# Kernel tuning notes

Hardware: AMD Instinct MI355X
Metric: run time of the kernel (lower is better)

## Reference

```python
import jax, jax.numpy as jnp
import numpy as np

SCALE = 1.0  # noise std used in the Gaussian log-pdf
HIGH = jax.lax.Precision.HIGHEST


def setup_inputs() -> dict:
    key = jax.random.key(0)
    k1, k2, k3 = jax.random.split(key, 3)
    B, N, D, T = 64, 256, 64, 4096
    data = jax.random.normal(k1, (B, N, D), dtype=jnp.float32)
    targets = jax.random.normal(k2, (B, N), dtype=jnp.float32)
    task_pool = jax.random.normal(k3, (T, D, 1), dtype=jnp.float32)
    return {"data": data, "targets": targets, "task_pool": task_pool}


def reference(data, targets, task_pool):
    # data: [B, N, D], targets: [B, N], task_pool: [T, D, 1]
    W = jnp.squeeze(task_pool).T  # [D, T]
    # Per-point, per-task Gaussian log-likelihood of targets under each task weight.
    Z = jnp.einsum('bnd,dt->bnt', data, W, precision=HIGH)  # [B, N, T]
    resid = targets[:, :, None] - Z
    logp = jax.scipy.stats.norm.logpdf(resid, loc=0.0, scale=SCALE)  # [B, N, T]
    # alpha for step i (i >= 1) is the cumulative log-lik over points 0..i-1.
    cum = jnp.cumsum(logp, axis=1)          # [B, N, T]
    alphas = cum[:, :-1]                    # [B, N-1, T], alphas[:, i-1] = alpha at step i
    post = jax.nn.softmax(alphas, axis=-1)  # posterior over tasks per step
    # MMSE weight per step: posterior-weighted average of task weights.
    w_mmse = jnp.einsum('bit,dt->bid', post, W, precision=HIGH)  # [B, N-1, D]
    preds_rest = jnp.einsum('bid,bid->bi', data[:, 1:], w_mmse)  # [B, N-1]
    # Step 0: prior mean weight (uniform average over task pool).
    pred0 = data[:, 0] @ W.mean(axis=1)  # [B]
    return jnp.concatenate([pred0[:, None], preds_rest], axis=1)  # [B, N]
```

## Files before the change

### kernel.cpp

```cpp
#include <hip/hip_runtime.h>
#include <math.h>

#define BB 64
#define NN 256
#define DD 64
#define TT 4096

#define NCH 16
#define CT (TT/NCH)
#define THREADS 512
#define WAVES 8
#define NB 32
#define NGRP (NN/NB)
#define BN (BB*NN)

#define NHL2E (-0.72134752044448170368f)

typedef __bf16 bf16x4 __attribute__((ext_vector_type(4)));
typedef __bf16 bf16x8 __attribute__((ext_vector_type(8)));
typedef float  f32x4  __attribute__((ext_vector_type(4)));

#define SHR1 0x111
#define SHR2 0x112
#define SHR4 0x114
#define SHR8 0x118

template<int C>
__device__ __forceinline__ float dppf(float x) {
  return __int_as_float(__builtin_amdgcn_update_dpp(
      0, __float_as_int(x), C, 0xf, 0xf, true));
}

__device__ __forceinline__ float bcast15(float x) {
  return __int_as_float(__builtin_amdgcn_ds_swizzle(__float_as_int(x), 0x1F0));
}

#define GLOAD_LDS16(gp, lp_) \
  __builtin_amdgcn_global_load_lds((const __attribute__((address_space(1))) void*)(gp), \
                                   (__attribute__((address_space(3))) void*)(lp_), 16, 0, 0)

__device__ __forceinline__ void merge32(const float2 (*sb)[NB], int lane,
                                        float2* __restrict__ part, size_t obase) {
  const int col = lane & 31;
  float2 p0 = sb[0][col];
  float M = p0.x, S = 1.f, V = p0.y;
  #pragma unroll
  for (int w = 1; w < WAVES; ++w) {
    float2 pw = sb[w][col];
    float mn = fmaxf(M, pw.x);
    float ea = __builtin_amdgcn_exp2f(M - mn);
    float eb = __builtin_amdgcn_exp2f(pw.x - mn);
    S = S * ea + eb;
    V = fmaf(V, ea, pw.y * eb);
    M = mn;
  }
  if (lane < 32) {
    float2 lr;
    lr.x = M + __log2f(S);
    lr.y = V / S;
    part[obase + (size_t)col * NCH] = lr;
  }
}

__global__ __launch_bounds__(THREADS, 4)
void mmse_phase1(const float* __restrict__ data,
                 const float* __restrict__ targets,
                 const float* __restrict__ Wp,
                 float2* __restrict__ part)
{
  const int bx   = blockIdx.x;
  const int b    = bx >> 4;
  const int ch   = bx & 15;
  const int tid  = threadIdx.x;
  const int lane = tid & 63;
  const int wave = tid >> 6;

  __shared__ uint4  dbufq[2][512];
  __shared__ float  tgl[NN];
  __shared__ float2 sbuf[2][WAVES][NB];

  unsigned char* dbufc = (unsigned char*)dbufq;

  bf16x8 aH[2][2], aL[2][2];
  {
    const int tb = ch * CT + wave * 32;
    #pragma unroll
    for (int tile = 0; tile < 2; ++tile) {
      #pragma unroll
      for (int s = 0; s < 2; ++s) {
        const int row = tb + tile * 16 + (lane & 15);
        const int kb  = s * 32 + (lane >> 4) * 8;
        const float* wp = Wp + (size_t)row * DD + kb;
        const float4 qa = *(const float4*)wp;
        const float4 qb = *(const float4*)(wp + 4);
        float f[8] = {qa.x, qa.y, qa.z, qa.w, qb.x, qb.y, qb.z, qb.w};
        bf16x8 hv, lv;
        #pragma unroll
        for (int j = 0; j < 8; ++j) {
          const __bf16 hj = (__bf16)f[j];
          hv[j] = hj;
          lv[j] = (__bf16)(f[j] - (float)hj);
        }
        aH[tile][s] = hv; aL[tile][s] = lv;
      }
    }
  }

  if (wave == 0)
    GLOAD_LDS16(targets + (size_t)b * NN + lane * 4, tgl);

  const float* __restrict__ dbase = data + (size_t)b * NN * DD;
  const int sn  = tid >> 4;
  const int sk8 = tid & 15;
  const int sphys = (sn * 128 + sk8 * 8) ^ ((sn & 7) << 4);

  {
    const float4 q = *(const float4*)(dbase + (size_t)sn * DD + sk8 * 4);
    float f[4] = {q.x, q.y, q.z, q.w};
    bf16x4 hv, lv;
    #pragma unroll
    for (int j = 0; j < 4; ++j) {
      const __bf16 hj = (__bf16)f[j];
      hv[j] = hj;
      lv[j] = (__bf16)(f[j] - (float)hj);
    }
    *(bf16x4*)(dbufc + sphys)        = hv;
    *(bf16x4*)(dbufc + 4096 + sphys) = lv;
  }
  __syncthreads();

  float c8[8];
  #pragma unroll
  for (int i = 0; i < 8; ++i) c8[i] = 0.f;

  const size_t obase0 = (size_t)(b * NN) * NCH + ch;
  const int ra = ((lane & 15) * 128 + (lane >> 4) * 16) ^ ((lane & 7) << 4);

  #pragma unroll 1
  for (int g = 0; g < NGRP; ++g) {
    const int buf = g & 1;
    const unsigned char* bp = dbufc + buf * 8192;

    float4 q;
    if (g + 1 < NGRP)
      q = *(const float4*)(dbase + (size_t)((g + 1) * NB + sn) * DD + sk8 * 4);

    if (g > 0 && wave == ((g - 1) & 7))
      merge32(sbuf[(g - 1) & 1], lane, part, obase0 + (size_t)((g - 1) * NB) * NCH);

    #pragma unroll
    for (int h = 0; h < 2; ++h) {
      const unsigned char* hp = bp + h * 2048;
      bf16x8 bh0 = *(const bf16x8*)(hp + ra);
      bf16x8 bh1 = *(const bf16x8*)(hp + (ra ^ 64));
      bf16x8 bl0 = *(const bf16x8*)(hp + 4096 + ra);
      bf16x8 bl1 = *(const bf16x8*)(hp + 4096 + (ra ^ 64));

      f32x4 zz[2];
      zz[0] = (f32x4)(0.f); zz[1] = (f32x4)(0.f);
      __builtin_amdgcn_s_setprio(1);
      zz[0] = __builtin_amdgcn_mfma_f32_16x16x32_bf16(aH[0][0], bh0, zz[0], 0, 0, 0);
      zz[0] = __builtin_amdgcn_mfma_f32_16x16x32_bf16(aH[0][0], bl0, zz[0], 0, 0, 0);
      zz[0] = __builtin_amdgcn_mfma_f32_16x16x32_bf16(aL[0][0], bh0, zz[0], 0, 0, 0);
      zz[0] = __builtin_amdgcn_mfma_f32_16x16x32_bf16(aH[0][1], bh1, zz[0], 0, 0, 0);
      zz[0] = __builtin_amdgcn_mfma_f32_16x16x32_bf16(aH[0][1], bl1, zz[0], 0, 0, 0);
      zz[0] = __builtin_amdgcn_mfma_f32_16x16x32_bf16(aL[0][1], bh1, zz[0], 0, 0, 0);
      zz[1] = __builtin_amdgcn_mfma_f32_16x16x32_bf16(aH[1][0], bh0, zz[1], 0, 0, 0);
      zz[1] = __builtin_amdgcn_mfma_f32_16x16x32_bf16(aH[1][0], bl0, zz[1], 0, 0, 0);
      zz[1] = __builtin_amdgcn_mfma_f32_16x16x32_bf16(aL[1][0], bh0, zz[1], 0, 0, 0);
      zz[1] = __builtin_amdgcn_mfma_f32_16x16x32_bf16(aH[1][1], bh1, zz[1], 0, 0, 0);
      zz[1] = __builtin_amdgcn_mfma_f32_16x16x32_bf16(aH[1][1], bl1, zz[1], 0, 0, 0);
      zz[1] = __builtin_amdgcn_mfma_f32_16x16x32_bf16(aL[1][1], bh1, zz[1], 0, 0, 0);
      __builtin_amdgcn_s_setprio(0);

      const float tgf = tgl[g * NB + h * 16 + (lane & 15)];

      float alpha[8];
      float mloc = -3.4e38f;
      #pragma unroll
      for (int tile = 0; tile < 2; ++tile) {
        #pragma unroll
        for (int r = 0; r < 4; ++r) {
          const int t8 = tile * 4 + r;
          const float z  = zz[tile][r];
          const float rr = tgf - z;
          const float lp = rr * rr * NHL2E;
          float x = lp;
          x += dppf<SHR1>(x);
          x += dppf<SHR2>(x);
          x += dppf<SHR4>(x);
          x += dppf<SHR8>(x);
          const float tot = bcast15(x);
          const float a_ = c8[t8] + (x - lp);
          alpha[t8] = a_;
          c8[t8] += tot;
          mloc = fmaxf(mloc, a_);
        }
      }
      float m = fmaxf(mloc, __shfl_xor(mloc, 16));
      m = fmaxf(m, __shfl_xor(m, 32));
      float sv = 0.f, vv = 0.f;
      #pragma unroll
      for (int tile = 0; tile < 2; ++tile) {
        #pragma unroll
        for (int r = 0; r < 4; ++r) {
          const float p = __builtin_amdgcn_exp2f(alpha[tile * 4 + r] - m);
          sv += p;
          vv = fmaf(p, zz[tile][r], vv);
        }
      }
      sv += __shfl_xor(sv, 16); sv += __shfl_xor(sv, 32);
      vv += __shfl_xor(vv, 16); vv += __shfl_xor(vv, 32);
      if (lane < 16) {
        float2 lr;
        lr.x = m + __log2f(sv);
        lr.y = vv / sv;
        sbuf[buf][wave][h * 16 + lane] = lr;
      }
    }

    if (g + 1 < NGRP) {
      float f[4] = {q.x, q.y, q.z, q.w};
      bf16x4 hv, lv;
      #pragma unroll
      for (int j = 0; j < 4; ++j) {
        const __bf16 hj = (__bf16)f[j];
        hv[j] = hj;
        lv[j] = (__bf16)(f[j] - (float)hj);
      }
      unsigned char* wb = dbufc + (buf ^ 1) * 8192;
      *(bf16x4*)(wb + sphys)        = hv;
      *(bf16x4*)(wb + 4096 + sphys) = lv;
    }
    __syncthreads();
  }

  if (wave == ((NGRP - 1) & 7))
    merge32(sbuf[(NGRP - 1) & 1], lane, part, obase0 + (size_t)((NGRP - 1) * NB) * NCH);
}

__global__ __launch_bounds__(256)
void mmse_phase2(const float* __restrict__ part, float* __restrict__ out)
{
  const int gid  = blockIdx.x * 256 + threadIdx.x;
  const int idx  = gid >> 1;
  const int half = gid & 1;
  const float2* __restrict__ p = (const float2*)part + (size_t)idx * NCH + half * 8;
  float M = -3.4e38f, S = 0.f, V = 0.f;
  #pragma unroll
  for (int c = 0; c < 8; ++c) {
    const float2 q = p[c];
    const float mn = fmaxf(M, q.x);
    const float ea = __builtin_amdgcn_exp2f(M - mn);
    const float eb = __builtin_amdgcn_exp2f(q.x - mn);
    S = fmaf(S, ea, eb);
    V = fmaf(V, ea, q.y * eb);
    M = mn;
  }
  const float m2 = __shfl_xor(M, 1), s2 = __shfl_xor(S, 1), v2 = __shfl_xor(V, 1);
  const float mn = fmaxf(M, m2);
  const float ea = __builtin_amdgcn_exp2f(M - mn);
  const float eb = __builtin_amdgcn_exp2f(m2 - mn);
  S = fmaf(S, ea, s2 * eb);
  V = fmaf(V, ea, v2 * eb);
  if (half == 0) out[idx] = V / S;
}

extern "C" void kernel_launch(void* const* d_in, const int* in_sizes, int n_in,
                              void* d_out, int out_size, void* d_ws, size_t ws_size,
                              hipStream_t stream)
{
  const float* data      = (const float*)d_in[0];
  const float* targets   = (const float*)d_in[1];
  const float* task_pool = (const float*)d_in[2];
  float* out = (float*)d_out;

  float2* part = (float2*)d_ws;

  hipLaunchKernelGGL(mmse_phase1, dim3(BB * NCH), dim3(THREADS), 0, stream,
                     data, targets, task_pool, part);
  hipLaunchKernelGGL(mmse_phase2, dim3(2 * BN / 256), dim3(256), 0, stream,
                     (const float*)part, out);
}
```

Before: 112.3 us.

## Double per-wave task tiles and halve task chunks to reuse staged data

Each wave now covers 64 tasks (four 16-row MFMA tiles) instead of 32, so each block handles 512 tasks and the grid shrinks from 1024 to 512 blocks. Each block still stages the same bf16 hi/lo data tiles, so the total data loading, splitting and LDS traffic across the grid halves, and the per-block merge overhead is spread over more tasks. Phase 2 is simplified to one thread per output merging 8 partials, with no shuffle. In exchange, register pressure rises (occupancy hint lowered from 4 to 3 blocks per CU) and fewer blocks give less parallelism to hide latency.

After: 120.8 us. 1.08x slower.

```diff
diff --git a/kernel.cpp b/kernel.cpp
--- a/kernel.cpp
+++ b/kernel.cpp
@@ -6,10 +6,11 @@
 #define DD 64
 #define TT 4096
 
-#define NCH 16
+#define NCH 8
 #define CT (TT/NCH)
 #define THREADS 512
 #define WAVES 8
+#define NTILE 4
 #define NB 32
 #define NGRP (NN/NB)
 #define BN (BB*NN)
@@ -62,15 +63,15 @@
   }
 }
 
-__global__ __launch_bounds__(THREADS, 4)
+__global__ __launch_bounds__(THREADS, 3)
 void mmse_phase1(const float* __restrict__ data,
                  const float* __restrict__ targets,
                  const float* __restrict__ Wp,
                  float2* __restrict__ part)
 {
   const int bx   = blockIdx.x;
-  const int b    = bx >> 4;
-  const int ch   = bx & 15;
+  const int b    = bx >> 3;
+  const int ch   = bx & 7;
   const int tid  = threadIdx.x;
   const int lane = tid & 63;
   const int wave = tid >> 6;
@@ -81,11 +82,11 @@
 
   unsigned char* dbufc = (unsigned char*)dbufq;
 
-  bf16x8 aH[2][2], aL[2][2];
+  bf16x8 aH[NTILE][2], aL[NTILE][2];
   {
-    const int tb = ch * CT + wave * 32;
+    const int tb = ch * CT + wave * 64;
     #pragma unroll
-    for (int tile = 0; tile < 2; ++tile) {
+    for (int tile = 0; tile < NTILE; ++tile) {
       #pragma unroll
       for (int s = 0; s < 2; ++s) {
         const int row = tb + tile * 16 + (lane & 15);
@@ -129,9 +130,9 @@
   }
   __syncthreads();
 
-  float c8[8];
+  float c16[16];
   #pragma unroll
-  for (int i = 0; i < 8; ++i) c8[i] = 0.f;
+  for (int i = 0; i < 16; ++i) c16[i] = 0.f;
 
   const size_t obase0 = (size_t)(b * NN) * NCH + ch;
   const int ra = ((lane & 15) * 128 + (lane >> 4) * 16) ^ ((lane & 7) << 4);
@@ -156,33 +157,30 @@
       bf16x8 bl0 = *(const bf16x8*)(hp + 4096 + ra);
       bf16x8 bl1 = *(const bf16x8*)(hp + 4096 + (ra ^ 64));
 
-      f32x4 zz[2];
-      zz[0] = (f32x4)(0.f); zz[1] = (f32x4)(0.f);
+      f32x4 zz[NTILE];
       __builtin_amdgcn_s_setprio(1);
-      zz[0] = __builtin_amdgcn_mfma_f32_16x16x32_bf16(aH[0][0], bh0, zz[0], 0, 0, 0);
-      zz[0] = __builtin_amdgcn_mfma_f32_16x16x32_bf16(aH[0][0], bl0, zz[0], 0, 0, 0);
-      zz[0] = __builtin_amdgcn_mfma_f32_16x16x32_bf16(aL[0][0], bh0, zz[0], 0, 0, 0);
-      zz[0] = __builtin_amdgcn_mfma_f32_16x16x32_bf16(aH[0][1], bh1, zz[0], 0, 0, 0);
-      zz[0] = __builtin_amdgcn_mfma_f32_16x16x32_bf16(aH[0][1], bl1, zz[0], 0, 0, 0);
-      zz[0] = __builtin_amdgcn_mfma_f32_16x16x32_bf16(aL[0][1], bh1, zz[0], 0, 0, 0);
-      zz[1] = __builtin_amdgcn_mfma_f32_16x16x32_bf16(aH[1][0], bh0, zz[1], 0, 0, 0);
-      zz[1] = __builtin_amdgcn_mfma_f32_16x16x32_bf16(aH[1][0], bl0, zz[1], 0, 0, 0);
-      zz[1] = __builtin_amdgcn_mfma_f32_16x16x32_bf16(aL[1][0], bh0, zz[1], 0, 0, 0);
-      zz[1] = __builtin_amdgcn_mfma_f32_16x16x32_bf16(aH[1][1], bh1, zz[1], 0, 0, 0);
-      zz[1] = __builtin_amdgcn_mfma_f32_16x16x32_bf16(aH[1][1], bl1, zz[1], 0, 0, 0);
-      zz[1] = __builtin_amdgcn_mfma_f32_16x16x32_bf16(aL[1][1], bh1, zz[1], 0, 0, 0);
+      #pragma unroll
+      for (int t = 0; t < NTILE; ++t) {
+        zz[t] = (f32x4)(0.f);
+        zz[t] = __builtin_amdgcn_mfma_f32_16x16x32_bf16(aH[t][0], bh0, zz[t], 0, 0, 0);
+        zz[t] = __builtin_amdgcn_mfma_f32_16x16x32_bf16(aH[t][0], bl0, zz[t], 0, 0, 0);
+        zz[t] = __builtin_amdgcn_mfma_f32_16x16x32_bf16(aL[t][0], bh0, zz[t], 0, 0, 0);
+        zz[t] = __builtin_amdgcn_mfma_f32_16x16x32_bf16(aH[t][1], bh1, zz[t], 0, 0, 0);
+        zz[t] = __builtin_amdgcn_mfma_f32_16x16x32_bf16(aH[t][1], bl1, zz[t], 0, 0, 0);
+        zz[t] = __builtin_amdgcn_mfma_f32_16x16x32_bf16(aL[t][1], bh1, zz[t], 0, 0, 0);
+      }
       __builtin_amdgcn_s_setprio(0);
 
       const float tgf = tgl[g * NB + h * 16 + (lane & 15)];
 
-      float alpha[8];
+      float alpha[16];
       float mloc = -3.4e38f;
       #pragma unroll
-      for (int tile = 0; tile < 2; ++tile) {
+      for (int t = 0; t < NTILE; ++t) {
         #pragma unroll
         for (int r = 0; r < 4; ++r) {
-          const int t8 = tile * 4 + r;
-          const float z  = zz[tile][r];
+          const int t16 = t * 4 + r;
+          const float z  = zz[t][r];
           const float rr = tgf - z;
           const float lp = rr * rr * NHL2E;
           float x = lp;
@@ -191,9 +189,9 @@
           x += dppf<SHR4>(x);
           x += dppf<SHR8>(x);
           const float tot = bcast15(x);
-          const float a_ = c8[t8] + (x - lp);
-          alpha[t8] = a_;
-          c8[t8] += tot;
+          const float a_ = c16[t16] + (x - lp);
+          alpha[t16] = a_;
+          c16[t16] += tot;
           mloc = fmaxf(mloc, a_);
         }
       }
@@ -201,12 +199,12 @@
       m = fmaxf(m, __shfl_xor(m, 32));
       float sv = 0.f, vv = 0.f;
       #pragma unroll
-      for (int tile = 0; tile < 2; ++tile) {
+      for (int t = 0; t < NTILE; ++t) {
         #pragma unroll
         for (int r = 0; r < 4; ++r) {
-          const float p = __builtin_amdgcn_exp2f(alpha[tile * 4 + r] - m);
+          const float p = __builtin_amdgcn_exp2f(alpha[t * 4 + r] - m);
           sv += p;
-          vv = fmaf(p, zz[tile][r], vv);
+          vv = fmaf(p, zz[t][r], vv);
         }
       }
       sv += __shfl_xor(sv, 16); sv += __shfl_xor(sv, 32);
@@ -240,15 +238,14 @@
 }
 
 __global__ __launch_bounds__(256)
-void mmse_phase2(const float* __restrict__ part, float* __restrict__ out)
+void mmse_phase2(const float2* __restrict__ part, float* __restrict__ out)
 {
-  const int gid  = blockIdx.x * 256 + threadIdx.x;
-  const int idx  = gid >> 1;
-  const int half = gid & 1;
-  const float2* __restrict__ p = (const float2*)part + (size_t)idx * NCH + half * 8;
-  float M = -3.4e38f, S = 0.f, V = 0.f;
+  const int idx = blockIdx.x * 256 + threadIdx.x;
+  const float2* __restrict__ p = part + (size_t)idx * NCH;
+  float2 q0 = p[0];
+  float M = q0.x, S = 1.f, V = q0.y;
   #pragma unroll
-  for (int c = 0; c < 8; ++c) {
+  for (int c = 1; c < NCH; ++c) {
     const float2 q = p[c];
     const float mn = fmaxf(M, q.x);
     const float ea = __builtin_amdgcn_exp2f(M - mn);
@@ -257,13 +254,7 @@
     V = fmaf(V, ea, q.y * eb);
     M = mn;
   }
-  const float m2 = __shfl_xor(M, 1), s2 = __shfl_xor(S, 1), v2 = __shfl_xor(V, 1);
-  const float mn = fmaxf(M, m2);
-  const float ea = __builtin_amdgcn_exp2f(M - mn);
-  const float eb = __builtin_amdgcn_exp2f(m2 - mn);
-  S = fmaf(S, ea, s2 * eb);
-  V = fmaf(V, ea, v2 * eb);
-  if (half == 0) out[idx] = V / S;
+  out[idx] = V / S;
 }
 
 extern "C" void kernel_launch(void* const* d_in, const int* in_sizes, int n_in,
@@ -279,6 +270,6 @@
 
   hipLaunchKernelGGL(mmse_phase1, dim3(BB * NCH), dim3(THREADS), 0, stream,
                      data, targets, task_pool, part);
-  hipLaunchKernelGGL(mmse_phase2, dim3(2 * BN / 256), dim3(256), 0, stream,
-                     (const float*)part, out);
-}
+  hipLaunchKernelGGL(mmse_phase2, dim3(BN / 256), dim3(256), 0, stream,
+                     part, out);
+}
```
